# Kernel tuning notes

Measured on AMD Instinct MI355X. Metric: run time of the kernel, lower is better.

## Reference

```python
import jax, jax.numpy as jnp
import numpy as np

N_EMBD = 768
N_HEAD = 8
B, T = 4, 2048

def setup_inputs() -> dict:
    key = jax.random.key(0)
    k1, k2, k3, k4, k5 = jax.random.split(key, 5)
    C = N_EMBD
    s = 1.0 / np.sqrt(C)
    return {
        "x": jax.random.normal(k1, (B, T, C), dtype=jnp.float32),
        "W_attn": jax.random.normal(k2, (C, 3 * C), dtype=jnp.float32) * s,
        "b_attn": jnp.zeros((3 * C,), dtype=jnp.float32),
        "W_proj": jax.random.normal(k3, (C, C), dtype=jnp.float32) * s,
        "b_proj": jnp.zeros((C,), dtype=jnp.float32),
    }

def reference(x, W_attn, b_attn, W_proj, b_proj):
    Bs, Ts, C = x.shape
    H = N_HEAD
    hs = C // H
    qkv = x @ W_attn + b_attn                      # [B,T,3C]
    q, k, v = jnp.split(qkv, 3, axis=-1)
    # reshape to [B,H,T,hs]
    q = q.reshape(Bs, Ts, H, hs).transpose(0, 2, 1, 3)
    k = k.reshape(Bs, Ts, H, hs).transpose(0, 2, 1, 3)
    v = v.reshape(Bs, Ts, H, hs).transpose(0, 2, 1, 3)
    scale = 1.0 / jnp.sqrt(jnp.float32(hs))
    att = jnp.einsum('bhid,bhjd->bhij', q, k) * scale   # [B,H,T,T]
    mask = jnp.tril(jnp.ones((Ts, Ts), dtype=bool))
    att = jnp.where(mask, att, -jnp.inf)
    m = jnp.max(att, axis=-1, keepdims=True)
    e = jnp.where(mask, jnp.exp(att - m), 0.0)
    # original kernel divides by (sum + 1e-9)
    att = e / (jnp.sum(e, axis=-1, keepdims=True) + 1e-9)
    y = jnp.einsum('bhij,bhjd->bhid', att, v)           # [B,H,T,hs]
    y = y.transpose(0, 2, 1, 3).reshape(Bs, Ts, C)
    return y @ W_proj + b_proj
```

## Files before the change

kernel.cpp:

```cpp
#include <hip/hip_runtime.h>

typedef __bf16 bf16;
typedef __attribute__((ext_vector_type(4))) __bf16 bf16x4;
typedef __attribute__((ext_vector_type(8))) __bf16 bf16x8;
typedef __attribute__((ext_vector_type(4))) float f32x4;

#define B_   4
#define T_   2048
#define C_   768
#define H_   8
#define HS_  96
#define M_   (B_ * T_)
#define QKN_ (3 * C_)

#define NEG_BIG (-1e30f)

#define KSTR 104
#define VSTR 72
#define PSTR 72

__device__ __forceinline__ void gload16(const bf16* gp, bf16* lp) {
    __builtin_amdgcn_global_load_lds(
        (const __attribute__((address_space(1))) unsigned int*)gp,
        (__attribute__((address_space(3))) unsigned int*)lp, 16, 0, 0);
}

__global__ void transpose_kernel(const float* __restrict__ W, bf16* __restrict__ Wt,
                                 int R, int Cn) {
    __shared__ bf16 tile[32][33];
    int tx = threadIdx.x, ty = threadIdx.y;
    int x  = blockIdx.x * 32 + tx;
    int y0 = blockIdx.y * 32;
#pragma unroll
    for (int j = 0; j < 32; j += 8)
        tile[ty + j][tx] = (bf16)W[(size_t)(y0 + ty + j) * Cn + x];
    __syncthreads();
    int y2 = blockIdx.x * 32;
    int x2 = y0 + tx;
#pragma unroll
    for (int j = 0; j < 32; j += 8)
        Wt[(size_t)(y2 + ty + j) * R + x2] = tile[tx][ty + j];
}

__global__ void f2b_kernel(const float* __restrict__ in, bf16* __restrict__ out) {
    int i = (blockIdx.x * 256 + threadIdx.x) * 4;
    f32x4 v = *(const f32x4*)&in[i];
    bf16x4 o = {(bf16)v[0], (bf16)v[1], (bf16)v[2], (bf16)v[3]};
    *(bf16x4*)&out[i] = o;
}

__global__ void v_transpose(const bf16* __restrict__ qkv, bf16* __restrict__ Vt) {
    __shared__ bf16 tile[32][33];
    int b = blockIdx.z;
    const bf16* src = qkv + (size_t)b * T_ * QKN_ + 2 * C_;
    bf16* dst = Vt + (size_t)b * C_ * T_;
    int tx = threadIdx.x, ty = threadIdx.y;
    int cc = blockIdx.x * 32;
    int tt = blockIdx.y * 32;
#pragma unroll
    for (int j = 0; j < 32; j += 8)
        tile[ty + j][tx] = src[(size_t)(tt + ty + j) * QKN_ + cc + tx];
    __syncthreads();
#pragma unroll
    for (int j = 0; j < 32; j += 8)
        dst[(size_t)(cc + ty + j) * T_ + tt + tx] = tile[tx][ty + j];
}

__global__ void sentinel_kernel(float* __restrict__ out, int n) {
    int i = blockIdx.x * 256 + threadIdx.x;
    if (i < n) out[i] = 12345.0f;
}

__device__ __forceinline__ void store1(bf16* p, float v)  { *p = (bf16)v; }
__device__ __forceinline__ void store1(float* p, float v) { *p = v; }

template <typename CT>
__global__ __launch_bounds__(256) void gemm_bt(const bf16* __restrict__ A,
                                               const bf16* __restrict__ Bt,
                                               const float* __restrict__ bias,
                                               CT* __restrict__ Cmat,
                                               int M, int N, int K) {
    __shared__ bf16 lda[128 * 64];
    __shared__ bf16 ldb[128 * 64];
    int tid  = threadIdx.x;
    int w    = tid >> 6;
    int lane = tid & 63;
    int col  = lane & 15, quad = lane >> 4;
    int wr   = w >> 1, wc = w & 1;
    int m0   = blockIdx.y * 128, n0 = blockIdx.x * 128;

    const f32x4 zero = {0.f, 0.f, 0.f, 0.f};
    f32x4 acc[4][4];
#pragma unroll
    for (int mr = 0; mr < 4; ++mr)
#pragma unroll
        for (int nc = 0; nc < 4; ++nc) acc[mr][nc] = zero;

    for (int k0 = 0; k0 < K; k0 += 64) {
#pragma unroll
        for (int i = 0; i < 4; ++i) {
            int gbase = i * 256 + w * 64;
            int g  = gbase + lane;
            int r  = g >> 3, cc = g & 7;
            gload16(&A[(size_t)(m0 + r) * K + k0 + cc * 8],  &lda[gbase * 8]);
            gload16(&Bt[(size_t)(n0 + r) * K + k0 + cc * 8], &ldb[gbase * 8]);
        }
        __syncthreads();
#pragma unroll
        for (int ks = 0; ks < 2; ++ks) {
            bf16x8 af[4], bfr[4];
#pragma unroll
            for (int t = 0; t < 4; ++t) {
                af[t]  = *(const bf16x8*)&lda[(wr * 64 + t * 16 + col) * 64 + ks * 32 + quad * 8];
                bfr[t] = *(const bf16x8*)&ldb[(wc * 64 + t * 16 + col) * 64 + ks * 32 + quad * 8];
            }
#pragma unroll
            for (int mr = 0; mr < 4; ++mr)
#pragma unroll
                for (int nc = 0; nc < 4; ++nc)
                    acc[mr][nc] = __builtin_amdgcn_mfma_f32_16x16x32_bf16(
                        af[mr], bfr[nc], acc[mr][nc], 0, 0, 0);
        }
        __syncthreads();
    }

#pragma unroll
    for (int nc = 0; nc < 4; ++nc) {
        int n = n0 + wc * 64 + nc * 16 + col;
        float bv = bias[n];
#pragma unroll
        for (int mr = 0; mr < 4; ++mr) {
#pragma unroll
            for (int r = 0; r < 4; ++r) {
                int row = m0 + wr * 64 + mr * 16 + quad * 4 + r;
                store1(&Cmat[(size_t)row * N + n], acc[mr][nc][r] + bv);
            }
        }
    }
}

__global__ __launch_bounds__(256) void attn_kernel(const bf16* __restrict__ qkv,
                                                   const bf16* __restrict__ Vt,
                                                   bf16* __restrict__ y,
                                                   int nGroups) {
    __shared__ bf16 ldsK[64 * KSTR];
    __shared__ bf16 ldsV[96 * VSTR];
    __shared__ bf16 ldsP[4 * 16 * PSTR];
    const int bid  = blockIdx.x;
    const int p    = bid / nGroups;
    const int g    = bid % nGroups;
    const int h    = g & 7, b = g >> 3;
    const int tid  = threadIdx.x;
    const int w    = tid >> 6, lane = tid & 63;
    const int col  = lane & 15, quad = lane >> 4;
    const float SCALE2 = 0.10206207261596577f * 1.4426950408889634f;
    const float M0 = 24.0f;
    const f32x4 zero = {0.f, 0.f, 0.f, 0.f};

    const bf16* qkvb = qkv + (size_t)b * T_ * QKN_;
    const bf16* Vtbh = Vt + (size_t)(b * H_ + h) * HS_ * T_;
    bf16* yb  = y + (size_t)b * T_ * C_;
    bf16* myP = &ldsP[w * 16 * PSTR];

#pragma unroll
    for (int half = 0; half < 2; ++half) {
        const int qt    = half ? p : (31 - p);
        const int rbase = qt * 64 + w * 16;

        bf16x8 qf[3];
#pragma unroll
        for (int c = 0; c < 3; ++c)
            qf[c] = *(const bf16x8*)&qkvb[(size_t)(rbase + col) * QKN_ + h * HS_ + c * 32 + quad * 8];

        f32x4 o[6];
#pragma unroll
        for (int n2 = 0; n2 < 6; ++n2) o[n2] = zero;
        float lsum = 0.f;

        const int njt = qt + 1;
        for (int jt = 0; jt < njt; ++jt) {
            int jb = jt * 64;
            __syncthreads();
#pragma unroll
            for (int i = 0; i < 3; ++i) {
                int chunk = i * 256 + tid;
                int r  = chunk / 12, cc = chunk - r * 12;
                *(bf16x8*)&ldsK[r * KSTR + cc * 8] =
                    *(const bf16x8*)&qkvb[(size_t)(jb + r) * QKN_ + C_ + h * HS_ + cc * 8];
                int r2 = chunk >> 3, c2 = chunk & 7;
                *(bf16x8*)&ldsV[r2 * VSTR + c2 * 8] =
                    *(const bf16x8*)&Vtbh[(size_t)r2 * T_ + jb + c2 * 8];
            }
            __syncthreads();

            bf16x8 kf[4][3];
#pragma unroll
            for (int nb = 0; nb < 4; ++nb)
#pragma unroll
                for (int c = 0; c < 3; ++c)
                    kf[nb][c] = *(const bf16x8*)&ldsK[(nb * 16 + col) * KSTR + c * 32 + quad * 8];

            f32x4 st[4];
#pragma unroll
            for (int nb = 0; nb < 4; ++nb) st[nb] = zero;
#pragma unroll
            for (int c = 0; c < 3; ++c)
#pragma unroll
                for (int nb = 0; nb < 4; ++nb)
                    st[nb] = __builtin_amdgcn_mfma_f32_16x16x32_bf16(
                        kf[nb][c], qf[c], st[nb], 0, 0, 0);

            if (jt == njt - 1) {
#pragma unroll
                for (int nb = 0; nb < 4; ++nb)
#pragma unroll
                    for (int r = 0; r < 4; ++r) {
                        int jg = jb + nb * 16 + quad * 4 + r;
                        st[nb][r] = (jg <= rbase + col) ? fmaf(st[nb][r], SCALE2, -M0)
                                                        : NEG_BIG;
                    }
            } else {
#pragma unroll
                for (int nb = 0; nb < 4; ++nb)
#pragma unroll
                    for (int r = 0; r < 4; ++r)
                        st[nb][r] = fmaf(st[nb][r], SCALE2, -M0);
            }

#pragma unroll
            for (int nb = 0; nb < 4; ++nb) {
#pragma unroll
                for (int r = 0; r < 4; ++r) {
                    float pv = exp2f(st[nb][r]);
                    st[nb][r] = pv;
                    lsum += pv;
                }
                bf16x4 pk = {(bf16)st[nb][0], (bf16)st[nb][1],
                             (bf16)st[nb][2], (bf16)st[nb][3]};
                *(bf16x4*)&myP[col * PSTR + nb * 16 + quad * 4] = pk;
            }

            bf16x8 vf[6][2];
#pragma unroll
            for (int n2 = 0; n2 < 6; ++n2)
#pragma unroll
                for (int c = 0; c < 2; ++c)
                    vf[n2][c] = *(const bf16x8*)&ldsV[(n2 * 16 + col) * VSTR + c * 32 + quad * 8];
            bf16x8 pa0 = *(const bf16x8*)&myP[col * PSTR + quad * 8];
            bf16x8 pa1 = *(const bf16x8*)&myP[col * PSTR + 32 + quad * 8];
#pragma unroll
            for (int n2 = 0; n2 < 6; ++n2)
                o[n2] = __builtin_amdgcn_mfma_f32_16x16x32_bf16(vf[n2][0], pa0, o[n2], 0, 0, 0);
#pragma unroll
            for (int n2 = 0; n2 < 6; ++n2)
                o[n2] = __builtin_amdgcn_mfma_f32_16x16x32_bf16(vf[n2][1], pa1, o[n2], 0, 0, 0);
        }

        lsum += __shfl_xor(lsum, 16, 64);
        lsum += __shfl_xor(lsum, 32, 64);
        float linv = 1.0f / lsum;
#pragma unroll
        for (int n2 = 0; n2 < 6; ++n2) {
            bf16x4 pk = {(bf16)(o[n2][0] * linv), (bf16)(o[n2][1] * linv),
                         (bf16)(o[n2][2] * linv), (bf16)(o[n2][3] * linv)};
            *(bf16x4*)&yb[(size_t)(rbase + col) * C_ + h * HS_ + n2 * 16 + quad * 4] = pk;
        }
    }
}

extern "C" void kernel_launch(void* const* d_in, const int* in_sizes, int n_in,
                              void* d_out, int out_size, void* d_ws, size_t ws_size,
                              hipStream_t stream) {
    (void)in_sizes; (void)n_in;
    const float* x      = (const float*)d_in[0];
    const float* W_attn = (const float*)d_in[1];
    const float* b_attn = (const float*)d_in[2];
    const float* W_proj = (const float*)d_in[3];
    const float* b_proj = (const float*)d_in[4];
    float* out = (float*)d_out;

    size_t e_wta = (size_t)QKN_ * C_;
    size_t e_wtp = (size_t)C_ * C_;
    size_t a_qkv = e_wta + e_wtp;
    size_t a_vt  = a_qkv + (size_t)M_ * QKN_;
    size_t a_yb  = a_vt + (size_t)M_ * C_;
    size_t needA = (a_yb + (size_t)M_ * C_) * sizeof(bf16);
    size_t b_qkv = e_wta + e_wtp;
    size_t b_vt  = b_qkv + (size_t)T_ * QKN_;
    size_t b_yb  = b_vt + (size_t)T_ * C_;
    size_t needB = (b_yb + (size_t)T_ * C_) * sizeof(bf16);

    if (ws_size >= needA) {
        bf16* Wt_attn = (bf16*)d_ws;
        bf16* Wt_proj = (bf16*)d_ws + e_wta;
        bf16* qkv     = (bf16*)d_ws + a_qkv;
        bf16* Vt      = (bf16*)d_ws + a_vt;
        bf16* yb      = (bf16*)d_ws + a_yb;
        bf16* xb = (bf16*)d_out;
        transpose_kernel<<<dim3(QKN_ / 32, C_ / 32), dim3(32, 8), 0, stream>>>(W_attn, Wt_attn, C_, QKN_);
        transpose_kernel<<<dim3(C_ / 32, C_ / 32), dim3(32, 8), 0, stream>>>(W_proj, Wt_proj, C_, C_);
        f2b_kernel<<<dim3(M_ * C_ / 1024), 256, 0, stream>>>(x, xb);
        gemm_bt<bf16><<<dim3(QKN_ / 128, M_ / 128), 256, 0, stream>>>(
            xb, Wt_attn, b_attn, qkv, M_, QKN_, C_);
        v_transpose<<<dim3(C_ / 32, T_ / 32, B_), dim3(32, 8), 0, stream>>>(qkv, Vt);
        attn_kernel<<<dim3(16 * H_ * B_), 256, 0, stream>>>(qkv, Vt, yb, H_ * B_);
        gemm_bt<float><<<dim3(C_ / 128, M_ / 128), 256, 0, stream>>>(
            yb, Wt_proj, b_proj, out, M_, C_, C_);
    } else if (ws_size >= needB) {
        bf16* Wt_attn = (bf16*)d_ws;
        bf16* Wt_proj = (bf16*)d_ws + e_wta;
        bf16* qkv     = (bf16*)d_ws + b_qkv;
        bf16* Vt      = (bf16*)d_ws + b_vt;
        bf16* yb      = (bf16*)d_ws + b_yb;
        transpose_kernel<<<dim3(QKN_ / 32, C_ / 32), dim3(32, 8), 0, stream>>>(W_attn, Wt_attn, C_, QKN_);
        transpose_kernel<<<dim3(C_ / 32, C_ / 32), dim3(32, 8), 0, stream>>>(W_proj, Wt_proj, C_, C_);
        for (int b = 0; b < B_; ++b) {
            const float* xsrc = x + (size_t)b * T_ * C_;
            float* outb       = out + (size_t)b * T_ * C_;
            bf16* xb          = (bf16*)outb;
            f2b_kernel<<<dim3(T_ * C_ / 1024), 256, 0, stream>>>(xsrc, xb);
            gemm_bt<bf16><<<dim3(QKN_ / 128, T_ / 128), 256, 0, stream>>>(
                xb, Wt_attn, b_attn, qkv, T_, QKN_, C_);
            v_transpose<<<dim3(C_ / 32, T_ / 32, 1), dim3(32, 8), 0, stream>>>(qkv, Vt);
            attn_kernel<<<dim3(16 * H_), 256, 0, stream>>>(qkv, Vt, yb, H_);
            gemm_bt<float><<<dim3(C_ / 128, T_ / 128), 256, 0, stream>>>(
                yb, Wt_proj, b_proj, outb, T_, C_, C_);
        }
    } else {
        sentinel_kernel<<<(out_size + 255) / 256, 256, 0, stream>>>(out, out_size);
    }
}
```

Baseline: 239.6 us.

## Fuse fp32 cast and V transpose into QKV GEMM, one query tile per attention block

```diff
diff --git a/kernel.cpp b/kernel.cpp
--- a/kernel.cpp
+++ b/kernel.cpp
@@ -42,44 +42,110 @@
         Wt[(size_t)(y2 + ty + j) * R + x2] = tile[tx][ty + j];
 }
 
-__global__ void f2b_kernel(const float* __restrict__ in, bf16* __restrict__ out) {
-    int i = (blockIdx.x * 256 + threadIdx.x) * 4;
-    f32x4 v = *(const f32x4*)&in[i];
-    bf16x4 o = {(bf16)v[0], (bf16)v[1], (bf16)v[2], (bf16)v[3]};
-    *(bf16x4*)&out[i] = o;
-}
-
-__global__ void v_transpose(const bf16* __restrict__ qkv, bf16* __restrict__ Vt) {
-    __shared__ bf16 tile[32][33];
-    int b = blockIdx.z;
-    const bf16* src = qkv + (size_t)b * T_ * QKN_ + 2 * C_;
-    bf16* dst = Vt + (size_t)b * C_ * T_;
-    int tx = threadIdx.x, ty = threadIdx.y;
-    int cc = blockIdx.x * 32;
-    int tt = blockIdx.y * 32;
-#pragma unroll
-    for (int j = 0; j < 32; j += 8)
-        tile[ty + j][tx] = src[(size_t)(tt + ty + j) * QKN_ + cc + tx];
-    __syncthreads();
-#pragma unroll
-    for (int j = 0; j < 32; j += 8)
-        dst[(size_t)(cc + ty + j) * T_ + tt + tx] = tile[tx][ty + j];
-}
-
 __global__ void sentinel_kernel(float* __restrict__ out, int n) {
     int i = blockIdx.x * 256 + threadIdx.x;
     if (i < n) out[i] = 12345.0f;
 }
 
-__device__ __forceinline__ void store1(bf16* p, float v)  { *p = (bf16)v; }
-__device__ __forceinline__ void store1(float* p, float v) { *p = v; }
-
-template <typename CT>
-__global__ __launch_bounds__(256) void gemm_bt(const bf16* __restrict__ A,
-                                               const bf16* __restrict__ Bt,
-                                               const float* __restrict__ bias,
-                                               CT* __restrict__ Cmat,
-                                               int M, int N, int K) {
+__device__ __forceinline__ bf16x8 load8f(const float* p) {
+    f32x4 v0 = *(const f32x4*)p;
+    f32x4 v1 = *(const f32x4*)(p + 4);
+    bf16x8 o;
+#pragma unroll
+    for (int i = 0; i < 4; ++i) { o[i] = (bf16)v0[i]; o[4 + i] = (bf16)v1[i]; }
+    return o;
+}
+
+__global__ __launch_bounds__(256) void gemm_qkv(const float* __restrict__ A,
+                                                const bf16* __restrict__ Bt,
+                                                const float* __restrict__ bias,
+                                                bf16* __restrict__ Cmat,
+                                                bf16* __restrict__ Vt,
+                                                int M, int N, int K) {
+    __shared__ bf16 lda[128 * 72];
+    __shared__ bf16 ldb[128 * 64];
+    int tid  = threadIdx.x;
+    int w    = tid >> 6;
+    int lane = tid & 63;
+    int col  = lane & 15, quad = lane >> 4;
+    int wr   = w >> 1, wc = w & 1;
+    int m0   = blockIdx.y * 128, n0 = blockIdx.x * 128;
+
+    const f32x4 zero = {0.f, 0.f, 0.f, 0.f};
+    f32x4 acc[4][4];
+#pragma unroll
+    for (int mr = 0; mr < 4; ++mr)
+#pragma unroll
+        for (int nc = 0; nc < 4; ++nc) acc[mr][nc] = zero;
+
+    for (int k0 = 0; k0 < K; k0 += 64) {
+#pragma unroll
+        for (int i = 0; i < 4; ++i) {
+            int chunk = i * 256 + tid;
+            int r = chunk >> 3, cc = chunk & 7;
+            *(bf16x8*)&lda[r * 72 + cc * 8] = load8f(&A[(size_t)(m0 + r) * K + k0 + cc * 8]);
+            int gbase = i * 256 + w * 64;
+            int gg = gbase + lane;
+            int rb = gg >> 3, cb = gg & 7;
+            gload16(&Bt[(size_t)(n0 + rb) * K + k0 + cb * 8], &ldb[gbase * 8]);
+        }
+        __syncthreads();
+#pragma unroll
+        for (int ks = 0; ks < 2; ++ks) {
+            bf16x8 af[4], bfr[4];
+#pragma unroll
+            for (int t = 0; t < 4; ++t) {
+                af[t]  = *(const bf16x8*)&lda[(wr * 64 + t * 16 + col) * 72 + ks * 32 + quad * 8];
+                bfr[t] = *(const bf16x8*)&ldb[(wc * 64 + t * 16 + col) * 64 + ks * 32 + quad * 8];
+            }
+#pragma unroll
+            for (int mr = 0; mr < 4; ++mr)
+#pragma unroll
+                for (int nc = 0; nc < 4; ++nc)
+                    acc[mr][nc] = __builtin_amdgcn_mfma_f32_16x16x32_bf16(
+                        af[mr], bfr[nc], acc[mr][nc], 0, 0, 0);
+        }
+        __syncthreads();
+    }
+
+#pragma unroll
+    for (int nc = 0; nc < 4; ++nc) {
+        int n = n0 + wc * 64 + nc * 16 + col;
+        float bv = bias[n];
+#pragma unroll
+        for (int mr = 0; mr < 4; ++mr) {
+#pragma unroll
+            for (int r = 0; r < 4; ++r) {
+                int row = m0 + wr * 64 + mr * 16 + quad * 4 + r;
+                Cmat[(size_t)row * N + n] = (bf16)(acc[mr][nc][r] + bv);
+            }
+        }
+    }
+    if (n0 >= 2 * C_) {
+        int batch = m0 >> 11;
+        bf16* Vtb = Vt + (size_t)batch * C_ * T_;
+        int t0 = (m0 & 2047) + wr * 64;
+#pragma unroll
+        for (int nc = 0; nc < 4; ++nc) {
+            int n  = n0 + wc * 64 + nc * 16 + col;
+            int vc = n - 2 * C_;
+            float bv = bias[n];
+#pragma unroll
+            for (int mr = 0; mr < 4; ++mr) {
+                int t = t0 + mr * 16 + quad * 4;
+                bf16x4 pk = {(bf16)(acc[mr][nc][0] + bv), (bf16)(acc[mr][nc][1] + bv),
+                             (bf16)(acc[mr][nc][2] + bv), (bf16)(acc[mr][nc][3] + bv)};
+                *(bf16x4*)&Vtb[(size_t)vc * T_ + t] = pk;
+            }
+        }
+    }
+}
+
+__global__ __launch_bounds__(256) void gemm_proj(const bf16* __restrict__ A,
+                                                 const bf16* __restrict__ Bt,
+                                                 const float* __restrict__ bias,
+                                                 float* __restrict__ Cmat,
+                                                 int M, int N, int K) {
     __shared__ bf16 lda[128 * 64];
     __shared__ bf16 ldb[128 * 64];
     int tid  = threadIdx.x;
@@ -133,7 +199,7 @@
 #pragma unroll
             for (int r = 0; r < 4; ++r) {
                 int row = m0 + wr * 64 + mr * 16 + quad * 4 + r;
-                store1(&Cmat[(size_t)row * N + n], acc[mr][nc][r] + bv);
+                Cmat[(size_t)row * N + n] = acc[mr][nc][r] + bv;
             }
         }
     }
@@ -147,7 +213,7 @@
     __shared__ bf16 ldsV[96 * VSTR];
     __shared__ bf16 ldsP[4 * 16 * PSTR];
     const int bid  = blockIdx.x;
-    const int p    = bid / nGroups;
+    const int qt   = 31 - bid / nGroups;
     const int g    = bid % nGroups;
     const int h    = g & 7, b = g >> 3;
     const int tid  = threadIdx.x;
@@ -162,109 +228,115 @@
     bf16* yb  = y + (size_t)b * T_ * C_;
     bf16* myP = &ldsP[w * 16 * PSTR];
 
-#pragma unroll
-    for (int half = 0; half < 2; ++half) {
-        const int qt    = half ? p : (31 - p);
-        const int rbase = qt * 64 + w * 16;
-
-        bf16x8 qf[3];
+    const int rbase = qt * 64 + w * 16;
+
+    bf16x8 qf[3];
+#pragma unroll
+    for (int c = 0; c < 3; ++c)
+        qf[c] = *(const bf16x8*)&qkvb[(size_t)(rbase + col) * QKN_ + h * HS_ + c * 32 + quad * 8];
+
+    const bf16* pK[3]; const bf16* pV[3];
+    bf16 *dK[3], *dV[3];
+#pragma unroll
+    for (int i = 0; i < 3; ++i) {
+        int chunk = i * 256 + tid;
+        int rK = chunk / 12, cK = chunk - rK * 12;
+        pK[i] = qkvb + (size_t)rK * QKN_ + C_ + h * HS_ + cK * 8;
+        dK[i] = &ldsK[rK * KSTR + cK * 8];
+        int rV = chunk >> 3, cV = chunk & 7;
+        pV[i] = Vtbh + (size_t)rV * T_ + cV * 8;
+        dV[i] = &ldsV[rV * VSTR + cV * 8];
+    }
+
+    f32x4 o[6];
+#pragma unroll
+    for (int n2 = 0; n2 < 6; ++n2) o[n2] = zero;
+    float lsum = 0.f;
+
+    const int njt = qt + 1;
+    for (int jt = 0; jt < njt; ++jt) {
+        int jb = jt * 64;
+        __syncthreads();
+#pragma unroll
+        for (int i = 0; i < 3; ++i) {
+            *(bf16x8*)dK[i] = *(const bf16x8*)pK[i];
+            *(bf16x8*)dV[i] = *(const bf16x8*)pV[i];
+            pK[i] += (size_t)64 * QKN_;
+            pV[i] += 64;
+        }
+        __syncthreads();
+
+        bf16x8 kf[4][3];
+#pragma unroll
+        for (int nb = 0; nb < 4; ++nb)
+#pragma unroll
+            for (int c = 0; c < 3; ++c)
+                kf[nb][c] = *(const bf16x8*)&ldsK[(nb * 16 + col) * KSTR + c * 32 + quad * 8];
+
+        f32x4 st[4];
+#pragma unroll
+        for (int nb = 0; nb < 4; ++nb) st[nb] = zero;
 #pragma unroll
         for (int c = 0; c < 3; ++c)
-            qf[c] = *(const bf16x8*)&qkvb[(size_t)(rbase + col) * QKN_ + h * HS_ + c * 32 + quad * 8];
-
-        f32x4 o[6];
-#pragma unroll
-        for (int n2 = 0; n2 < 6; ++n2) o[n2] = zero;
-        float lsum = 0.f;
-
-        const int njt = qt + 1;
-        for (int jt = 0; jt < njt; ++jt) {
-            int jb = jt * 64;
-            __syncthreads();
-#pragma unroll
-            for (int i = 0; i < 3; ++i) {
-                int chunk = i * 256 + tid;
-                int r  = chunk / 12, cc = chunk - r * 12;
-                *(bf16x8*)&ldsK[r * KSTR + cc * 8] =
-                    *(const bf16x8*)&qkvb[(size_t)(jb + r) * QKN_ + C_ + h * HS_ + cc * 8];
-                int r2 = chunk >> 3, c2 = chunk & 7;
-                *(bf16x8*)&ldsV[r2 * VSTR + c2 * 8] =
-                    *(const bf16x8*)&Vtbh[(size_t)r2 * T_ + jb + c2 * 8];
-            }
-            __syncthreads();
-
-            bf16x8 kf[4][3];
 #pragma unroll
             for (int nb = 0; nb < 4; ++nb)
-#pragma unroll
-                for (int c = 0; c < 3; ++c)
-                    kf[nb][c] = *(const bf16x8*)&ldsK[(nb * 16 + col) * KSTR + c * 32 + quad * 8];
-
-            f32x4 st[4];
-#pragma unroll
-            for (int nb = 0; nb < 4; ++nb) st[nb] = zero;
-#pragma unroll
-            for (int c = 0; c < 3; ++c)
-#pragma unroll
-                for (int nb = 0; nb < 4; ++nb)
-                    st[nb] = __builtin_amdgcn_mfma_f32_16x16x32_bf16(
-                        kf[nb][c], qf[c], st[nb], 0, 0, 0);
-
-            if (jt == njt - 1) {
-#pragma unroll
-                for (int nb = 0; nb < 4; ++nb)
-#pragma unroll
-                    for (int r = 0; r < 4; ++r) {
-                        int jg = jb + nb * 16 + quad * 4 + r;
-                        st[nb][r] = (jg <= rbase + col) ? fmaf(st[nb][r], SCALE2, -M0)
-                                                        : NEG_BIG;
-                    }
-            } else {
-#pragma unroll
-                for (int nb = 0; nb < 4; ++nb)
-#pragma unroll
-                    for (int r = 0; r < 4; ++r)
-                        st[nb][r] = fmaf(st[nb][r], SCALE2, -M0);
-            }
-
-#pragma unroll
-            for (int nb = 0; nb < 4; ++nb) {
+                st[nb] = __builtin_amdgcn_mfma_f32_16x16x32_bf16(
+                    kf[nb][c], qf[c], st[nb], 0, 0, 0);
+
+        if (jt == njt - 1) {
+#pragma unroll
+            for (int nb = 0; nb < 4; ++nb)
 #pragma unroll
                 for (int r = 0; r < 4; ++r) {
-                    float pv = exp2f(st[nb][r]);
-                    st[nb][r] = pv;
-                    lsum += pv;
+                    int jg = jb + nb * 16 + quad * 4 + r;
+                    st[nb][r] = (jg <= rbase + col) ? fmaf(st[nb][r], SCALE2, -M0)
+                                                    : NEG_BIG;
                 }
-                bf16x4 pk = {(bf16)st[nb][0], (bf16)st[nb][1],
-                             (bf16)st[nb][2], (bf16)st[nb][3]};
-                *(bf16x4*)&myP[col * PSTR + nb * 16 + quad * 4] = pk;
-            }
-
-            bf16x8 vf[6][2];
-#pragma unroll
-            for (int n2 = 0; n2 < 6; ++n2)
-#pragma unroll
-                for (int c = 0; c < 2; ++c)
-                    vf[n2][c] = *(const bf16x8*)&ldsV[(n2 * 16 + col) * VSTR + c * 32 + quad * 8];
-            bf16x8 pa0 = *(const bf16x8*)&myP[col * PSTR + quad * 8];
-            bf16x8 pa1 = *(const bf16x8*)&myP[col * PSTR + 32 + quad * 8];
-#pragma unroll
-            for (int n2 = 0; n2 < 6; ++n2)
-                o[n2] = __builtin_amdgcn_mfma_f32_16x16x32_bf16(vf[n2][0], pa0, o[n2], 0, 0, 0);
-#pragma unroll
-            for (int n2 = 0; n2 < 6; ++n2)
-                o[n2] = __builtin_amdgcn_mfma_f32_16x16x32_bf16(vf[n2][1], pa1, o[n2], 0, 0, 0);
-        }
-
-        lsum += __shfl_xor(lsum, 16, 64);
-        lsum += __shfl_xor(lsum, 32, 64);
-        float linv = 1.0f / lsum;
-#pragma unroll
-        for (int n2 = 0; n2 < 6; ++n2) {
-            bf16x4 pk = {(bf16)(o[n2][0] * linv), (bf16)(o[n2][1] * linv),
-                         (bf16)(o[n2][2] * linv), (bf16)(o[n2][3] * linv)};
-            *(bf16x4*)&yb[(size_t)(rbase + col) * C_ + h * HS_ + n2 * 16 + quad * 4] = pk;
-        }
+        } else {
+#pragma unroll
+            for (int nb = 0; nb < 4; ++nb)
+#pragma unroll
+                for (int r = 0; r < 4; ++r)
+                    st[nb][r] = fmaf(st[nb][r], SCALE2, -M0);
+        }
+
+#pragma unroll
+        for (int nb = 0; nb < 4; ++nb) {
+#pragma unroll
+            for (int r = 0; r < 4; ++r) {
+                float pv = exp2f(st[nb][r]);
+                st[nb][r] = pv;
+                lsum += pv;
+            }
+            bf16x4 pk = {(bf16)st[nb][0], (bf16)st[nb][1],
+                         (bf16)st[nb][2], (bf16)st[nb][3]};
+            *(bf16x4*)&myP[col * PSTR + nb * 16 + quad * 4] = pk;
+        }
+
+        bf16x8 vf[6][2];
+#pragma unroll
+        for (int n2 = 0; n2 < 6; ++n2)
+#pragma unroll
+            for (int c = 0; c < 2; ++c)
+                vf[n2][c] = *(const bf16x8*)&ldsV[(n2 * 16 + col) * VSTR + c * 32 + quad * 8];
+        bf16x8 pa0 = *(const bf16x8*)&myP[col * PSTR + quad * 8];
+        bf16x8 pa1 = *(const bf16x8*)&myP[col * PSTR + 32 + quad * 8];
+#pragma unroll
+        for (int n2 = 0; n2 < 6; ++n2)
+            o[n2] = __builtin_amdgcn_mfma_f32_16x16x32_bf16(vf[n2][0], pa0, o[n2], 0, 0, 0);
+#pragma unroll
+        for (int n2 = 0; n2 < 6; ++n2)
+            o[n2] = __builtin_amdgcn_mfma_f32_16x16x32_bf16(vf[n2][1], pa1, o[n2], 0, 0, 0);
+    }
+
+    lsum += __shfl_xor(lsum, 16, 64);
+    lsum += __shfl_xor(lsum, 32, 64);
+    float linv = 1.0f / lsum;
+#pragma unroll
+    for (int n2 = 0; n2 < 6; ++n2) {
+        bf16x4 pk = {(bf16)(o[n2][0] * linv), (bf16)(o[n2][1] * linv),
+                     (bf16)(o[n2][2] * linv), (bf16)(o[n2][3] * linv)};
+        *(bf16x4*)&yb[(size_t)(rbase + col) * C_ + h * HS_ + n2 * 16 + quad * 4] = pk;
     }
 }
 
@@ -296,15 +368,12 @@
         bf16* qkv     = (bf16*)d_ws + a_qkv;
         bf16* Vt      = (bf16*)d_ws + a_vt;
         bf16* yb      = (bf16*)d_ws + a_yb;
-        bf16* xb = (bf16*)d_out;
         transpose_kernel<<<dim3(QKN_ / 32, C_ / 32), dim3(32, 8), 0, stream>>>(W_attn, Wt_attn, C_, QKN_);
         transpose_kernel<<<dim3(C_ / 32, C_ / 32), dim3(32, 8), 0, stream>>>(W_proj, Wt_proj, C_, C_);
-        f2b_kernel<<<dim3(M_ * C_ / 1024), 256, 0, stream>>>(x, xb);
-        gemm_bt<bf16><<<dim3(QKN_ / 128, M_ / 128), 256, 0, stream>>>(
-            xb, Wt_attn, b_attn, qkv, M_, QKN_, C_);
-        v_transpose<<<dim3(C_ / 32, T_ / 32, B_), dim3(32, 8), 0, stream>>>(qkv, Vt);
-        attn_kernel<<<dim3(16 * H_ * B_), 256, 0, stream>>>(qkv, Vt, yb, H_ * B_);
-        gemm_bt<float><<<dim3(C_ / 128, M_ / 128), 256, 0, stream>>>(
+        gemm_qkv<<<dim3(QKN_ / 128, M_ / 128), 256, 0, stream>>>(
+            x, Wt_attn, b_attn, qkv, Vt, M_, QKN_, C_);
+        attn_kernel<<<dim3(32 * H_ * B_), 256, 0, stream>>>(qkv, Vt, yb, H_ * B_);
+        gemm_proj<<<dim3(C_ / 128, M_ / 128), 256, 0, stream>>>(
             yb, Wt_proj, b_proj, out, M_, C_, C_);
     } else if (ws_size >= needB) {
         bf16* Wt_attn = (bf16*)d_ws;
@@ -315,15 +384,12 @@
         transpose_kernel<<<dim3(QKN_ / 32, C_ / 32), dim3(32, 8), 0, stream>>>(W_attn, Wt_attn, C_, QKN_);
         transpose_kernel<<<dim3(C_ / 32, C_ / 32), dim3(32, 8), 0, stream>>>(W_proj, Wt_proj, C_, C_);
         for (int b = 0; b < B_; ++b) {
-            const float* xsrc = x + (size_t)b * T_ * C_;
-            float* outb       = out + (size_t)b * T_ * C_;
-            bf16* xb          = (bf16*)outb;
-            f2b_kernel<<<dim3(T_ * C_ / 1024), 256, 0, stream>>>(xsrc, xb);
-            gemm_bt<bf16><<<dim3(QKN_ / 128, T_ / 128), 256, 0, stream>>>(
-                xb, Wt_attn, b_attn, qkv, T_, QKN_, C_);
-            v_transpose<<<dim3(C_ / 32, T_ / 32, 1), dim3(32, 8), 0, stream>>>(qkv, Vt);
-            attn_kernel<<<dim3(16 * H_), 256, 0, stream>>>(qkv, Vt, yb, H_);
-            gemm_bt<float><<<dim3(C_ / 128, T_ / 128), 256, 0, stream>>>(
+            const float* xb = x + (size_t)b * T_ * C_;
+            float* outb     = out + (size_t)b * T_ * C_;
+            gemm_qkv<<<dim3(QKN_ / 128, T_ / 128), 256, 0, stream>>>(
+                xb, Wt_attn, b_attn, qkv, Vt, T_, QKN_, C_);
+            attn_kernel<<<dim3(32 * H_), 256, 0, stream>>>(qkv, Vt, yb, H_);
+            gemm_proj<<<dim3(C_ / 128, T_ / 128), 256, 0, stream>>>(
                 yb, Wt_proj, b_proj, outb, T_, C_, C_);
         }
     } else {
```

Measured after the change: 234.3 us. 1.02x faster.
